# Kernel tuning notes

Measured on AMD Instinct MI355X. Metric: run time of the kernel, lower is better.

## Reference

```python
import jax, jax.numpy as jnp
import numpy as np

K = 7          # involution kernel size
GC = 16        # group_channels (hardcoded in module)
BN_EPS = 1e-5
LN_EPS = 1e-6


def _forward(x, conv1_w, conv1_b, bn_gamma, bn_beta, bn_mean, bn_var,
             conv2_w, conv2_b, ln_w, ln_b, w1, b1, w2, b2):
    b, c, h, w = x.shape
    groups = c // GC
    # --- involution: dynamic kernel generation (1x1 conv -> BN(eval) -> ReLU -> 1x1 conv) ---
    t = jnp.einsum('bchw,oc->bohw', x, conv1_w) + conv1_b[None, :, None, None]
    t = (t - bn_mean[None, :, None, None]) * (bn_gamma / jnp.sqrt(bn_var + BN_EPS))[None, :, None, None] \
        + bn_beta[None, :, None, None]
    t = jax.nn.relu(t)
    wgt = jnp.einsum('bchw,oc->bohw', t, conv2_w) + conv2_b[None, :, None, None]
    wgt = wgt.reshape(b, groups, K * K, h, w)                  # (b,g,k2,h,w)
    # --- unfold: gather kxk neighborhoods (channel-major, then kh, kw — matches torch Unfold) ---
    p = (K - 1) // 2
    xp = jnp.pad(x, ((0, 0), (0, 0), (p, p), (p, p)))
    patches = jnp.stack([xp[:, :, i:i + h, j:j + w]
                         for i in range(K) for j in range(K)], axis=2)   # (b,c,k2,h,w)
    patches = patches.reshape(b, groups, GC, K * K, h, w)
    # weighted sum over kernel positions
    out = jnp.einsum('bgkhw,bgckhw->bgchw', wgt, patches).reshape(b, c, h, w)
    # --- LN + MLP residual (channels_last) ---
    y = out.transpose(0, 2, 3, 1)                               # (b,h,w,c)
    mu = y.mean(-1, keepdims=True)
    var = ((y - mu) ** 2).mean(-1, keepdims=True)
    y = (y - mu) / jnp.sqrt(var + LN_EPS) * ln_w + ln_b
    y = jax.nn.gelu(y @ w1.T + b1, approximate=False)           # torch GELU = exact erf
    y = y @ w2.T + b2                                           # dropout_rate=0 -> identity
    return y.transpose(0, 3, 1, 2) + x


def setup_inputs() -> dict:
    key = jax.random.key(0)
    ks = jax.random.split(key, 6)
    dim = 128
    groups = dim // GC
    red = dim // 4
    b, h, w = 8, 56, 56
    return {
        'x': jax.random.normal(ks[0], (b, dim, h, w), jnp.float32),
        'conv1_w': jax.random.normal(ks[1], (red, dim), jnp.float32) * (1.0 / np.sqrt(dim)),
        'conv1_b': jnp.zeros((red,), jnp.float32),
        'bn_gamma': jnp.ones((red,), jnp.float32),
        'bn_beta': jnp.zeros((red,), jnp.float32),
        'bn_mean': jnp.zeros((red,), jnp.float32),
        'bn_var': jnp.ones((red,), jnp.float32),
        'conv2_w': jax.random.normal(ks[2], (K * K * groups, red), jnp.float32) * (1.0 / np.sqrt(red)),
        'conv2_b': jnp.zeros((K * K * groups,), jnp.float32),
        'ln_w': jnp.ones((dim,), jnp.float32),
        'ln_b': jnp.zeros((dim,), jnp.float32),
        'w1': jax.random.normal(ks[3], (4 * dim, dim), jnp.float32) * (1.0 / np.sqrt(dim)),
        'b1': jnp.zeros((4 * dim,), jnp.float32),
        'w2': jax.random.normal(ks[4], (dim, 4 * dim), jnp.float32) * (1.0 / np.sqrt(4 * dim)),
        'b2': jnp.zeros((dim,), jnp.float32),
    }


def reference(x, conv1_w, conv1_b, bn_gamma, bn_beta, bn_mean, bn_var,
              conv2_w, conv2_b, ln_w, ln_b, w1, b1, w2, b2):
    return _forward(x, conv1_w, conv1_b, bn_gamma, bn_beta, bn_mean, bn_var,
                    conv2_w, conv2_b, ln_w, ln_b, w1, b1, w2, b2)
```

## Files before the change

### kernel.cpp

```cpp
#include <hip/hip_runtime.h>
#include <hip/hip_bf16.h>
#include <math.h>

#define HW    3136
#define WIMG  56
#define NPIX  25088
#define CIN   128
#define RED   32
#define NGROUP 8
#define GCH   16
#define KKK   49

typedef __attribute__((ext_vector_type(8))) short short8;
typedef __attribute__((ext_vector_type(4))) float f32x4;
typedef unsigned short ushort_t;

static __device__ __forceinline__ unsigned int f2b(float f) {
    union { __hip_bfloat16 b; unsigned short u; } cv;
    cv.b = __float2bfloat16(f);
    return (unsigned int)cv.u;
}

static __device__ __forceinline__ float gelu_t(float h) {
    float z = h * fmaf(0.0356774081f, h * h, 0.7978845608f);
    float e = __expf(-2.f * z);
    return __fdividef(h, 1.f + e);
}

__global__ __launch_bounds__(256) void k_prep(const float* __restrict__ conv1_w,
    const float* __restrict__ conv1_b, const float* __restrict__ bn_g,
    const float* __restrict__ bn_b, const float* __restrict__ bn_m,
    const float* __restrict__ bn_v, const float* __restrict__ conv2_w,
    const float* __restrict__ ln_w, const float* __restrict__ w1,
    const float* __restrict__ w2,
    ushort_t* __restrict__ c1b, ushort_t* __restrict__ c2b,
    ushort_t* __restrict__ lw1b, ushort_t* __restrict__ w2b,
    float* __restrict__ sc1, float* __restrict__ sh1)
{
    int id = blockIdx.x * 256 + threadIdx.x;
    w2b[id] = (ushort_t)f2b(w2[id]);
    int c = id & 127;
    lw1b[id] = (ushort_t)f2b(w1[id] * ln_w[c]);
    if (id < 4096)  c1b[id] = (ushort_t)f2b(conv1_w[id]);
    if (id < 12800) c2b[id] = (id < 12544) ? (ushort_t)f2b(conv2_w[id]) : (ushort_t)0;
    if (id < 32) {
        float sc = bn_g[id] * rsqrtf(bn_v[id] + 1e-5f);
        sc1[id] = sc;
        sh1[id] = (conv1_b[id] - bn_m[id]) * sc + bn_b[id];
    }
}

__global__ void k_prep2(const float* __restrict__ w1, const float* __restrict__ ln_w,
    const float* __restrict__ ln_b, const float* __restrict__ b1,
    float* __restrict__ s1, float* __restrict__ t1)
{
    int n = threadIdx.x;
    const float* wr = w1 + (size_t)n * 128;
    float s = 0.f, t = 0.f;
    #pragma unroll 8
    for (int c = 0; c < 128; ++c) { float w = wr[c]; s += ln_w[c] * w; t += ln_b[c] * w; }
    s1[n] = s; t1[n] = t + b1[n];
}

__global__ __launch_bounds__(256) void k_dw(const float* __restrict__ x,
    const short* __restrict__ c1b, const short* __restrict__ c2b,
    const float* __restrict__ sc1, const float* __restrict__ sh1,
    const float* __restrict__ c2bias, ushort_t* __restrict__ wgtT)
{
    __shared__ short sxa[64 * 136];
    __shared__ short st[64 * 40];
    int tid = threadIdx.x;
    int P0 = blockIdx.x * 64;
    int b  = P0 / HW;
    int p0 = P0 - b * HW;
    const float* xb = x + (size_t)b * CIN * HW + p0;
    #pragma unroll
    for (int it = 0; it < 32; ++it) {
        int idx = it * 256 + tid;
        int c = idx >> 6, pp = idx & 63;
        sxa[pp * 136 + c] = (short)f2b(xb[(size_t)c * HW + pp]);
    }
    __syncthreads();
    int lane = tid & 63, wv = tid >> 6;
    int ln15 = lane & 15, quad = lane >> 4;

    f32x4 acc1[2] = {(f32x4)0.f, (f32x4)0.f};
    #pragma unroll
    for (int kc = 0; kc < 128; kc += 32) {
        short8 af = *(const short8*)&sxa[(wv * 16 + ln15) * 136 + kc + quad * 8];
        #pragma unroll
        for (int nt = 0; nt < 2; ++nt) {
            short8 bf = *(const short8*)&c1b[(size_t)(nt * 16 + ln15) * 128 + kc + quad * 8];
            acc1[nt] = __builtin_amdgcn_mfma_f32_16x16x32_bf16(af, bf, acc1[nt], 0, 0, 0);
        }
    }
    #pragma unroll
    for (int nt = 0; nt < 2; ++nt) {
        int o = nt * 16 + ln15;
        float sc = sc1[o], sh = sh1[o];
        #pragma unroll
        for (int r = 0; r < 4; ++r) {
            float tv = fmaxf(acc1[nt][r] * sc + sh, 0.f);
            st[(wv * 16 + quad * 4 + r) * 40 + o] = (short)f2b(tv);
        }
    }
    short8 af2 = *(const short8*)&st[(wv * 16 + ln15) * 40 + quad * 8];
    f32x4 zc = (f32x4)0.f;
    #pragma unroll
    for (int nt = 0; nt < 25; ++nt) {
        int gk = nt * 16 + ln15;
        short8 bf2 = *(const short8*)&c2b[(size_t)gk * 32 + quad * 8];
        f32x4 a2 = __builtin_amdgcn_mfma_f32_16x16x32_bf16(af2, bf2, zc, 0, 0, 0);
        if (gk < 392) {
            float bj = c2bias[gk];
            uint2 pk;
            pk.x = f2b(a2[0] + bj) | (f2b(a2[1] + bj) << 16);
            pk.y = f2b(a2[2] + bj) | (f2b(a2[3] + bj) << 16);
            *(uint2*)&wgtT[(size_t)gk * NPIX + P0 + wv * 16 + quad * 4] = pk;
        }
    }
}

__global__ __launch_bounds__(256) void k_inv(const float* __restrict__ x,
    const ushort_t* __restrict__ wgtT, ushort_t* __restrict__ invb)
{
    int id  = blockIdx.x * 256 + threadIdx.x;
    int gy  = id / 6272;
    int q   = id - gy * 6272;
    int g   = gy >> 1;
    int sub = gy & 1;
    int P0  = q * 4;
    int b   = P0 / HW;
    int p   = P0 - b * HW;
    int prow = p / WIMG;
    int pcol = p - prow * WIMG;
    const float* xc = x + ((size_t)b * CIN + g * GCH + sub * 8) * HW;
    const ushort_t* wg = wgtT + (size_t)g * KKK * NPIX + P0;
    float acc[4][8];
    #pragma unroll
    for (int i = 0; i < 4; ++i)
        #pragma unroll
        for (int c = 0; c < 8; ++c) acc[i][c] = 0.f;
    bool c_lo = (pcol >= 4);
    bool c_hi = (pcol <= 48);
    #pragma unroll
    for (int dy = -3; dy <= 3; ++dy) {
        int grow = prow + dy;
        if (grow < 0 || grow >= WIMG) continue;
        float wkf[7][4];
        #pragma unroll
        for (int dx = 0; dx < 7; ++dx) {
            uint2 wld = *(const uint2*)&wg[(size_t)((dy + 3) * 7 + dx) * NPIX];
            wkf[dx][0] = __uint_as_float(wld.x << 16);
            wkf[dx][1] = __uint_as_float(wld.x & 0xffff0000u);
            wkf[dx][2] = __uint_as_float(wld.y << 16);
            wkf[dx][3] = __uint_as_float(wld.y & 0xffff0000u);
        }
        const float* xrow = xc + grow * WIMG + pcol;
        #pragma unroll
        for (int c = 0; c < 8; ++c) {
            const float* xr = xrow + (size_t)c * HW;
            float4 v0 = c_lo ? *(const float4*)(xr - 4) : make_float4(0.f,0.f,0.f,0.f);
            float4 v1 = *(const float4*)(xr);
            float4 v2 = c_hi ? *(const float4*)(xr + 4) : make_float4(0.f,0.f,0.f,0.f);
            float vv[12] = {v0.x,v0.y,v0.z,v0.w, v1.x,v1.y,v1.z,v1.w, v2.x,v2.y,v2.z,v2.w};
            #pragma unroll
            for (int dx = 0; dx < 7; ++dx)
                #pragma unroll
                for (int i = 0; i < 4; ++i)
                    acc[i][c] += wkf[dx][i] * vv[i + dx + 1];
        }
    }
    #pragma unroll
    for (int i = 0; i < 4; ++i) {
        unsigned pk[4];
        #pragma unroll
        for (int h = 0; h < 4; ++h)
            pk[h] = f2b(acc[i][2*h]) | (f2b(acc[i][2*h+1]) << 16);
        *(uint4*)&invb[(size_t)(P0 + i) * CIN + g * GCH + sub * 8] = make_uint4(pk[0],pk[1],pk[2],pk[3]);
    }
}

__global__ __launch_bounds__(256) void k_stats(const ushort_t* __restrict__ invb,
    float* __restrict__ ssum, float* __restrict__ ssq)
{
    int p = blockIdx.x * 256 + threadIdx.x;
    const uint4* row = (const uint4*)(invb + (size_t)p * CIN);
    float s = 0.f, s2 = 0.f;
    #pragma unroll
    for (int i = 0; i < 16; ++i) {
        uint4 v = row[i];
        unsigned u[4] = {v.x, v.y, v.z, v.w};
        #pragma unroll
        for (int j = 0; j < 4; ++j) {
            float f0 = __uint_as_float(u[j] << 16);
            float f1 = __uint_as_float(u[j] & 0xffff0000u);
            s += f0 + f1;
            s2 += f0 * f0 + f1 * f1;
        }
    }
    ssum[p] = s; ssq[p] = s2;
}

__global__ __launch_bounds__(256) void k_mlp(const ushort_t* __restrict__ invb,
    const ushort_t* __restrict__ lw1b, const ushort_t* __restrict__ w2b,
    const float* __restrict__ ssum, const float* __restrict__ ssq,
    const float* __restrict__ s1, const float* __restrict__ t1,
    const float* __restrict__ b2, const float* __restrict__ xres,
    float* __restrict__ outp)
{
    __shared__ short sx[64 * 136];
    __shared__ short sh[64 * 136];
    __shared__ float sls[512], slt[512];
    int tid = threadIdx.x;
    int P0  = blockIdx.x * 64;

    #pragma unroll
    for (int it = 0; it < 4; ++it) {
        int idx = it * 256 + tid;
        int row = idx >> 4, ch = idx & 15;
        *(uint4*)&sx[row * 136 + ch * 8] =
            *(const uint4*)&invb[(size_t)(P0 + row) * 128 + ch * 8];
    }
    sls[tid] = s1[tid]; sls[tid + 256] = s1[tid + 256];
    slt[tid] = t1[tid]; slt[tid + 256] = t1[tid + 256];
    __syncthreads();

    int lane = tid & 63, wv = tid >> 6;
    int ln15 = lane & 15, quad = lane >> 4;

    float mu_r[4], rs_r[4];
    #pragma unroll
    for (int tn = 0; tn < 4; ++tn) {
        int p = P0 + tn * 16 + ln15;
        float m = ssum[p] * (1.f / 128.f);
        float v = ssq[p] * (1.f / 128.f) - m * m;
        mu_r[tn] = m; rs_r[tn] = rsqrtf(v + 1e-6f);
    }

    f32x4 acc2[4][2];
    #pragma unroll
    for (int i = 0; i < 4; ++i)
        #pragma unroll
        for (int j = 0; j < 2; ++j) acc2[i][j] = (f32x4)0.f;

    for (int j = 0; j < 4; ++j) {
        f32x4 acc1[2][4];
        #pragma unroll
        for (int tm = 0; tm < 2; ++tm)
            #pragma unroll
            for (int tn = 0; tn < 4; ++tn) acc1[tm][tn] = (f32x4)0.f;
        #pragma unroll
        for (int kc = 0; kc < 128; kc += 32) {
            short8 af[2], bf[4];
            #pragma unroll
            for (int tm = 0; tm < 2; ++tm)
                af[tm] = *(const short8*)&lw1b[(size_t)(j * 128 + wv * 32 + tm * 16 + ln15) * 128 + kc + quad * 8];
            #pragma unroll
            for (int tn = 0; tn < 4; ++tn)
                bf[tn] = *(const short8*)&sx[(tn * 16 + ln15) * 136 + kc + quad * 8];
            #pragma unroll
            for (int tm = 0; tm < 2; ++tm)
                #pragma unroll
                for (int tn = 0; tn < 4; ++tn)
                    acc1[tm][tn] = __builtin_amdgcn_mfma_f32_16x16x32_bf16(af[tm], bf[tn], acc1[tm][tn], 0, 0, 0);
        }
        #pragma unroll
        for (int tn = 0; tn < 4; ++tn) {
            int px = tn * 16 + ln15;
            #pragma unroll
            for (int tm = 0; tm < 2; ++tm) {
                int nl = wv * 32 + tm * 16 + quad * 4;
                int n  = j * 128 + nl;
                float g0 = gelu_t(rs_r[tn] * (acc1[tm][tn][0] - mu_r[tn] * sls[n + 0]) + slt[n + 0]);
                float g1 = gelu_t(rs_r[tn] * (acc1[tm][tn][1] - mu_r[tn] * sls[n + 1]) + slt[n + 1]);
                float g2 = gelu_t(rs_r[tn] * (acc1[tm][tn][2] - mu_r[tn] * sls[n + 2]) + slt[n + 2]);
                float g3 = gelu_t(rs_r[tn] * (acc1[tm][tn][3] - mu_r[tn] * sls[n + 3]) + slt[n + 3]);
                uint2 pk;
                pk.x = f2b(g0) | (f2b(g1) << 16);
                pk.y = f2b(g2) | (f2b(g3) << 16);
                *(uint2*)&sh[px * 136 + nl] = pk;
            }
        }
        __syncthreads();
        #pragma unroll
        for (int kc = 0; kc < 128; kc += 32) {
            short8 af[4], bf[2];
            #pragma unroll
            for (int tm = 0; tm < 4; ++tm)
                af[tm] = *(const short8*)&sh[(tm * 16 + ln15) * 136 + kc + quad * 8];
            #pragma unroll
            for (int tn = 0; tn < 2; ++tn)
                bf[tn] = *(const short8*)&w2b[(size_t)(wv * 32 + tn * 16 + ln15) * 512 + j * 128 + kc + quad * 8];
            #pragma unroll
            for (int tm = 0; tm < 4; ++tm)
                #pragma unroll
                for (int tn = 0; tn < 2; ++tn)
                    acc2[tm][tn] = __builtin_amdgcn_mfma_f32_16x16x32_bf16(af[tm], bf[tn], acc2[tm][tn], 0, 0, 0);
        }
        __syncthreads();
    }

    int b = P0 / HW, p0i = P0 - b * HW;
    #pragma unroll
    for (int tm = 0; tm < 4; ++tm) {
        int p = p0i + tm * 16 + quad * 4;
        #pragma unroll
        for (int tn = 0; tn < 2; ++tn) {
            int c = wv * 32 + tn * 16 + ln15;
            size_t base = ((size_t)b * CIN + c) * HW + p;
            float bj = b2[c];
            float4 rv = *(const float4*)&xres[base];
            float4 ov = make_float4(acc2[tm][tn][0] + bj + rv.x,
                                    acc2[tm][tn][1] + bj + rv.y,
                                    acc2[tm][tn][2] + bj + rv.z,
                                    acc2[tm][tn][3] + bj + rv.w);
            *(float4*)&outp[base] = ov;
        }
    }
}

extern "C" void kernel_launch(void* const* d_in, const int* in_sizes, int n_in,
                              void* d_out, int out_size, void* d_ws, size_t ws_size,
                              hipStream_t stream) {
    const float* x       = (const float*)d_in[0];
    const float* conv1_w = (const float*)d_in[1];
    const float* conv1_b = (const float*)d_in[2];
    const float* bn_g    = (const float*)d_in[3];
    const float* bn_b    = (const float*)d_in[4];
    const float* bn_m    = (const float*)d_in[5];
    const float* bn_v    = (const float*)d_in[6];
    const float* conv2_w = (const float*)d_in[7];
    const float* conv2_b = (const float*)d_in[8];
    const float* ln_w    = (const float*)d_in[9];
    const float* ln_b    = (const float*)d_in[10];
    const float* w1      = (const float*)d_in[11];
    const float* b1      = (const float*)d_in[12];
    const float* w2      = (const float*)d_in[13];
    const float* b2      = (const float*)d_in[14];
    float* out = (float*)d_out;

    float* F = (float*)d_ws;
    float* ssum = F;
    float* ssq  = F + 25088;
    float* sc1  = F + 50176;
    float* sh1  = F + 50208;
    float* s1   = F + 50240;
    float* t1   = F + 50752;
    ushort_t* S    = (ushort_t*)(F + 51264);
    ushort_t* wgtT = S;
    ushort_t* invb = S + 9834496;
    ushort_t* c1b  = invb + 3211264;
    ushort_t* c2b  = c1b + 4096;
    ushort_t* lw1b = c2b + 12800;
    ushort_t* w2b  = lw1b + 65536;

    k_prep <<<256, 256, 0, stream>>>(conv1_w, conv1_b, bn_g, bn_b, bn_m, bn_v,
                                     conv2_w, ln_w, w1, w2, c1b, c2b, lw1b, w2b, sc1, sh1);
    k_prep2<<<1, 512, 0, stream>>>(w1, ln_w, ln_b, b1, s1, t1);
    k_dw   <<<392, 256, 0, stream>>>(x, (const short*)c1b, (const short*)c2b,
                                     sc1, sh1, conv2_b, wgtT);
    k_inv  <<<392, 256, 0, stream>>>(x, wgtT, invb);
    k_stats<<<98, 256, 0, stream>>>(invb, ssum, ssq);
    k_mlp  <<<392, 256, 0, stream>>>(invb, lw1b, w2b, ssum, ssq, s1, t1, b2, x, out);
}
```

Before: 172.8 us.

## Fuse kernel-gen, involution, LN stats and MLP into one megakernel

Merges the dynamic-weight generation, involution, LayerNorm statistics and MLP kernels into a single per-64-pixel-tile kernel. The generated weights and involution outputs stay in shared memory, so the large global intermediates (wgtT, invb, ssum/ssq) and three launches go away. LN statistics are reduced in shared memory from fp32 accumulators instead of being reread from bf16. The cost is about 78KB of shared memory per block, which lowers occupancy, and the involution stage of each block now runs serially before the MLP stage.

New measurement: 149.9 us. 1.15x faster.

```diff
diff --git a/kernel.cpp b/kernel.cpp
--- a/kernel.cpp
+++ b/kernel.cpp
@@ -62,45 +62,57 @@
     s1[n] = s; t1[n] = t + b1[n];
 }
 
-__global__ __launch_bounds__(256) void k_dw(const float* __restrict__ x,
+__global__ __launch_bounds__(256) void k_mega(const float* __restrict__ x,
     const short* __restrict__ c1b, const short* __restrict__ c2b,
     const float* __restrict__ sc1, const float* __restrict__ sh1,
-    const float* __restrict__ c2bias, ushort_t* __restrict__ wgtT)
+    const float* __restrict__ c2bias,
+    const ushort_t* __restrict__ lw1b, const ushort_t* __restrict__ w2b,
+    const float* __restrict__ s1, const float* __restrict__ t1,
+    const float* __restrict__ b2, float* __restrict__ outp)
 {
-    __shared__ short sxa[64 * 136];
-    __shared__ short st[64 * 40];
-    int tid = threadIdx.x;
-    int P0 = blockIdx.x * 64;
-    int b  = P0 / HW;
-    int p0 = P0 - b * HW;
-    const float* xb = x + (size_t)b * CIN * HW + p0;
+    __shared__ __align__(16) char smem[79936];
+    short* swg  = (short*)smem;
+    short* sh   = (short*)smem;
+    short* sx   = (short*)smem + 26656;
+    short* st   = (short*)(smem + 70720);
+    float* sred  = (float*)(smem + 70720);
+    float* sred2 = sred + 1088;
+    float* smu   = sred2 + 1088;
+    float* srs   = smu + 64;
+
+    int tid  = threadIdx.x;
+    int P0   = blockIdx.x * 64;
+    int b    = P0 / HW;
+    int p0i  = P0 - b * HW;
+    int lane = tid & 63, wv = tid >> 6;
+    int ln15 = lane & 15, quad = lane >> 4;
+
+    const float* xb = x + (size_t)b * CIN * HW + p0i;
     #pragma unroll
     for (int it = 0; it < 32; ++it) {
         int idx = it * 256 + tid;
         int c = idx >> 6, pp = idx & 63;
-        sxa[pp * 136 + c] = (short)f2b(xb[(size_t)c * HW + pp]);
+        sx[pp * 136 + c] = (short)f2b(xb[(size_t)c * HW + pp]);
     }
     __syncthreads();
-    int lane = tid & 63, wv = tid >> 6;
-    int ln15 = lane & 15, quad = lane >> 4;
-
-    f32x4 acc1[2] = {(f32x4)0.f, (f32x4)0.f};
+
+    f32x4 acc1c[2] = {(f32x4)0.f, (f32x4)0.f};
     #pragma unroll
     for (int kc = 0; kc < 128; kc += 32) {
-        short8 af = *(const short8*)&sxa[(wv * 16 + ln15) * 136 + kc + quad * 8];
+        short8 af = *(const short8*)&sx[(wv * 16 + ln15) * 136 + kc + quad * 8];
         #pragma unroll
         for (int nt = 0; nt < 2; ++nt) {
             short8 bf = *(const short8*)&c1b[(size_t)(nt * 16 + ln15) * 128 + kc + quad * 8];
-            acc1[nt] = __builtin_amdgcn_mfma_f32_16x16x32_bf16(af, bf, acc1[nt], 0, 0, 0);
+            acc1c[nt] = __builtin_amdgcn_mfma_f32_16x16x32_bf16(af, bf, acc1c[nt], 0, 0, 0);
         }
     }
     #pragma unroll
     for (int nt = 0; nt < 2; ++nt) {
         int o = nt * 16 + ln15;
-        float sc = sc1[o], sh = sh1[o];
+        float sc = sc1[o], shv = sh1[o];
         #pragma unroll
         for (int r = 0; r < 4; ++r) {
-            float tv = fmaxf(acc1[nt][r] * sc + sh, 0.f);
+            float tv = fmaxf(acc1c[nt][r] * sc + shv, 0.f);
             st[(wv * 16 + quad * 4 + r) * 40 + o] = (short)f2b(tv);
         }
     }
@@ -116,126 +128,90 @@
             uint2 pk;
             pk.x = f2b(a2[0] + bj) | (f2b(a2[1] + bj) << 16);
             pk.y = f2b(a2[2] + bj) | (f2b(a2[3] + bj) << 16);
-            *(uint2*)&wgtT[(size_t)gk * NPIX + P0 + wv * 16 + quad * 4] = pk;
-        }
-    }
-}
-
-__global__ __launch_bounds__(256) void k_inv(const float* __restrict__ x,
-    const ushort_t* __restrict__ wgtT, ushort_t* __restrict__ invb)
-{
-    int id  = blockIdx.x * 256 + threadIdx.x;
-    int gy  = id / 6272;
-    int q   = id - gy * 6272;
-    int g   = gy >> 1;
-    int sub = gy & 1;
-    int P0  = q * 4;
-    int b   = P0 / HW;
-    int p   = P0 - b * HW;
-    int prow = p / WIMG;
-    int pcol = p - prow * WIMG;
-    const float* xc = x + ((size_t)b * CIN + g * GCH + sub * 8) * HW;
-    const ushort_t* wg = wgtT + (size_t)g * KKK * NPIX + P0;
-    float acc[4][8];
-    #pragma unroll
-    for (int i = 0; i < 4; ++i)
-        #pragma unroll
-        for (int c = 0; c < 8; ++c) acc[i][c] = 0.f;
-    bool c_lo = (pcol >= 4);
-    bool c_hi = (pcol <= 48);
-    #pragma unroll
-    for (int dy = -3; dy <= 3; ++dy) {
-        int grow = prow + dy;
-        if (grow < 0 || grow >= WIMG) continue;
-        float wkf[7][4];
-        #pragma unroll
-        for (int dx = 0; dx < 7; ++dx) {
-            uint2 wld = *(const uint2*)&wg[(size_t)((dy + 3) * 7 + dx) * NPIX];
-            wkf[dx][0] = __uint_as_float(wld.x << 16);
-            wkf[dx][1] = __uint_as_float(wld.x & 0xffff0000u);
-            wkf[dx][2] = __uint_as_float(wld.y << 16);
-            wkf[dx][3] = __uint_as_float(wld.y & 0xffff0000u);
-        }
-        const float* xrow = xc + grow * WIMG + pcol;
-        #pragma unroll
-        for (int c = 0; c < 8; ++c) {
-            const float* xr = xrow + (size_t)c * HW;
-            float4 v0 = c_lo ? *(const float4*)(xr - 4) : make_float4(0.f,0.f,0.f,0.f);
-            float4 v1 = *(const float4*)(xr);
-            float4 v2 = c_hi ? *(const float4*)(xr + 4) : make_float4(0.f,0.f,0.f,0.f);
-            float vv[12] = {v0.x,v0.y,v0.z,v0.w, v1.x,v1.y,v1.z,v1.w, v2.x,v2.y,v2.z,v2.w};
-            #pragma unroll
-            for (int dx = 0; dx < 7; ++dx)
+            *(uint2*)&swg[gk * 68 + wv * 16 + quad * 4] = pk;
+        }
+    }
+    __syncthreads();
+
+    {
+        int q   = tid & 15;
+        int gy  = tid >> 4;
+        int g   = gy >> 1;
+        int sub = gy & 1;
+        int pl0 = q * 4;
+        int p   = p0i + pl0;
+        int prow = p / WIMG;
+        int pcol = p - prow * WIMG;
+        const float* xc = x + ((size_t)b * CIN + g * GCH + sub * 8) * HW;
+        float acc[4][8];
+        #pragma unroll
+        for (int i = 0; i < 4; ++i)
+            #pragma unroll
+            for (int c = 0; c < 8; ++c) acc[i][c] = 0.f;
+        bool c_lo = (pcol >= 4);
+        bool c_hi = (pcol <= 48);
+        #pragma unroll
+        for (int dy = -3; dy <= 3; ++dy) {
+            int grow = prow + dy;
+            if (grow < 0 || grow >= WIMG) continue;
+            float wkf[7][4];
+            #pragma unroll
+            for (int dx = 0; dx < 7; ++dx) {
+                int gk = g * KKK + (dy + 3) * 7 + dx;
+                uint2 wld = *(const uint2*)&swg[gk * 68 + pl0];
+                wkf[dx][0] = __uint_as_float(wld.x << 16);
+                wkf[dx][1] = __uint_as_float(wld.x & 0xffff0000u);
+                wkf[dx][2] = __uint_as_float(wld.y << 16);
+                wkf[dx][3] = __uint_as_float(wld.y & 0xffff0000u);
+            }
+            const float* xrow = xc + grow * WIMG + pcol;
+            #pragma unroll
+            for (int c = 0; c < 8; ++c) {
+                const float* xr = xrow + (size_t)c * HW;
+                float4 v0 = c_lo ? *(const float4*)(xr - 4) : make_float4(0.f,0.f,0.f,0.f);
+                float4 v1 = *(const float4*)(xr);
+                float4 v2 = c_hi ? *(const float4*)(xr + 4) : make_float4(0.f,0.f,0.f,0.f);
+                float vv[12] = {v0.x,v0.y,v0.z,v0.w, v1.x,v1.y,v1.z,v1.w, v2.x,v2.y,v2.z,v2.w};
                 #pragma unroll
-                for (int i = 0; i < 4; ++i)
-                    acc[i][c] += wkf[dx][i] * vv[i + dx + 1];
-        }
-    }
-    #pragma unroll
-    for (int i = 0; i < 4; ++i) {
-        unsigned pk[4];
-        #pragma unroll
-        for (int h = 0; h < 4; ++h)
-            pk[h] = f2b(acc[i][2*h]) | (f2b(acc[i][2*h+1]) << 16);
-        *(uint4*)&invb[(size_t)(P0 + i) * CIN + g * GCH + sub * 8] = make_uint4(pk[0],pk[1],pk[2],pk[3]);
-    }
-}
-
-__global__ __launch_bounds__(256) void k_stats(const ushort_t* __restrict__ invb,
-    float* __restrict__ ssum, float* __restrict__ ssq)
-{
-    int p = blockIdx.x * 256 + threadIdx.x;
-    const uint4* row = (const uint4*)(invb + (size_t)p * CIN);
-    float s = 0.f, s2 = 0.f;
-    #pragma unroll
-    for (int i = 0; i < 16; ++i) {
-        uint4 v = row[i];
-        unsigned u[4] = {v.x, v.y, v.z, v.w};
-        #pragma unroll
-        for (int j = 0; j < 4; ++j) {
-            float f0 = __uint_as_float(u[j] << 16);
-            float f1 = __uint_as_float(u[j] & 0xffff0000u);
-            s += f0 + f1;
-            s2 += f0 * f0 + f1 * f1;
-        }
-    }
-    ssum[p] = s; ssq[p] = s2;
-}
-
-__global__ __launch_bounds__(256) void k_mlp(const ushort_t* __restrict__ invb,
-    const ushort_t* __restrict__ lw1b, const ushort_t* __restrict__ w2b,
-    const float* __restrict__ ssum, const float* __restrict__ ssq,
-    const float* __restrict__ s1, const float* __restrict__ t1,
-    const float* __restrict__ b2, const float* __restrict__ xres,
-    float* __restrict__ outp)
-{
-    __shared__ short sx[64 * 136];
-    __shared__ short sh[64 * 136];
-    __shared__ float sls[512], slt[512];
-    int tid = threadIdx.x;
-    int P0  = blockIdx.x * 64;
-
-    #pragma unroll
-    for (int it = 0; it < 4; ++it) {
-        int idx = it * 256 + tid;
-        int row = idx >> 4, ch = idx & 15;
-        *(uint4*)&sx[row * 136 + ch * 8] =
-            *(const uint4*)&invb[(size_t)(P0 + row) * 128 + ch * 8];
-    }
-    sls[tid] = s1[tid]; sls[tid + 256] = s1[tid + 256];
-    slt[tid] = t1[tid]; slt[tid + 256] = t1[tid + 256];
+                for (int dx = 0; dx < 7; ++dx)
+                    #pragma unroll
+                    for (int i = 0; i < 4; ++i)
+                        acc[i][c] += wkf[dx][i] * vv[i + dx + 1];
+            }
+        }
+        #pragma unroll
+        for (int i = 0; i < 4; ++i) {
+            unsigned pk[4];
+            float s = 0.f, s2 = 0.f;
+            #pragma unroll
+            for (int h = 0; h < 4; ++h)
+                pk[h] = f2b(acc[i][2*h]) | (f2b(acc[i][2*h+1]) << 16);
+            #pragma unroll
+            for (int c = 0; c < 8; ++c) { s += acc[i][c]; s2 += acc[i][c] * acc[i][c]; }
+            *(uint4*)&sx[(pl0 + i) * 136 + g * 16 + sub * 8] = make_uint4(pk[0],pk[1],pk[2],pk[3]);
+            sred [(pl0 + i) * 17 + gy] = s;
+            sred2[(pl0 + i) * 17 + gy] = s2;
+        }
+    }
     __syncthreads();
 
-    int lane = tid & 63, wv = tid >> 6;
-    int ln15 = lane & 15, quad = lane >> 4;
+    if (tid < 64) {
+        float s = 0.f, s2 = 0.f;
+        #pragma unroll
+        for (int gy = 0; gy < 16; ++gy) { s += sred[tid * 17 + gy]; s2 += sred2[tid * 17 + gy]; }
+        float m = s * (1.f / 128.f);
+        float v = s2 * (1.f / 128.f) - m * m;
+        smu[tid] = m;
+        srs[tid] = rsqrtf(v + 1e-6f);
+    }
+    __syncthreads();
 
     float mu_r[4], rs_r[4];
     #pragma unroll
     for (int tn = 0; tn < 4; ++tn) {
-        int p = P0 + tn * 16 + ln15;
-        float m = ssum[p] * (1.f / 128.f);
-        float v = ssq[p] * (1.f / 128.f) - m * m;
-        mu_r[tn] = m; rs_r[tn] = rsqrtf(v + 1e-6f);
+        int px = tn * 16 + ln15;
+        mu_r[tn] = smu[px];
+        rs_r[tn] = srs[px];
     }
 
     f32x4 acc2[4][2];
@@ -266,16 +242,18 @@
                     acc1[tm][tn] = __builtin_amdgcn_mfma_f32_16x16x32_bf16(af[tm], bf[tn], acc1[tm][tn], 0, 0, 0);
         }
         #pragma unroll
-        for (int tn = 0; tn < 4; ++tn) {
-            int px = tn * 16 + ln15;
-            #pragma unroll
-            for (int tm = 0; tm < 2; ++tm) {
-                int nl = wv * 32 + tm * 16 + quad * 4;
-                int n  = j * 128 + nl;
-                float g0 = gelu_t(rs_r[tn] * (acc1[tm][tn][0] - mu_r[tn] * sls[n + 0]) + slt[n + 0]);
-                float g1 = gelu_t(rs_r[tn] * (acc1[tm][tn][1] - mu_r[tn] * sls[n + 1]) + slt[n + 1]);
-                float g2 = gelu_t(rs_r[tn] * (acc1[tm][tn][2] - mu_r[tn] * sls[n + 2]) + slt[n + 2]);
-                float g3 = gelu_t(rs_r[tn] * (acc1[tm][tn][3] - mu_r[tn] * sls[n + 3]) + slt[n + 3]);
+        for (int tm = 0; tm < 2; ++tm) {
+            int nl = wv * 32 + tm * 16 + quad * 4;
+            int n  = j * 128 + nl;
+            float4 s14 = *(const float4*)&s1[n];
+            float4 t14 = *(const float4*)&t1[n];
+            #pragma unroll
+            for (int tn = 0; tn < 4; ++tn) {
+                int px = tn * 16 + ln15;
+                float g0 = gelu_t(rs_r[tn] * (acc1[tm][tn][0] - mu_r[tn] * s14.x) + t14.x);
+                float g1 = gelu_t(rs_r[tn] * (acc1[tm][tn][1] - mu_r[tn] * s14.y) + t14.y);
+                float g2 = gelu_t(rs_r[tn] * (acc1[tm][tn][2] - mu_r[tn] * s14.z) + t14.z);
+                float g3 = gelu_t(rs_r[tn] * (acc1[tm][tn][3] - mu_r[tn] * s14.w) + t14.w);
                 uint2 pk;
                 pk.x = f2b(g0) | (f2b(g1) << 16);
                 pk.y = f2b(g2) | (f2b(g3) << 16);
@@ -301,7 +279,6 @@
         __syncthreads();
     }
 
-    int b = P0 / HW, p0i = P0 - b * HW;
     #pragma unroll
     for (int tm = 0; tm < 4; ++tm) {
         int p = p0i + tm * 16 + quad * 4;
@@ -310,7 +287,7 @@
             int c = wv * 32 + tn * 16 + ln15;
             size_t base = ((size_t)b * CIN + c) * HW + p;
             float bj = b2[c];
-            float4 rv = *(const float4*)&xres[base];
+            float4 rv = *(const float4*)&x[base];
             float4 ov = make_float4(acc2[tm][tn][0] + bj + rv.x,
                                     acc2[tm][tn][1] + bj + rv.y,
                                     acc2[tm][tn][2] + bj + rv.z,
@@ -341,16 +318,12 @@
     float* out = (float*)d_out;
 
     float* F = (float*)d_ws;
-    float* ssum = F;
-    float* ssq  = F + 25088;
-    float* sc1  = F + 50176;
-    float* sh1  = F + 50208;
-    float* s1   = F + 50240;
-    float* t1   = F + 50752;
-    ushort_t* S    = (ushort_t*)(F + 51264);
-    ushort_t* wgtT = S;
-    ushort_t* invb = S + 9834496;
-    ushort_t* c1b  = invb + 3211264;
+    float* sc1  = F;
+    float* sh1  = F + 32;
+    float* s1   = F + 64;
+    float* t1   = F + 576;
+    ushort_t* S    = (ushort_t*)(F + 1088);
+    ushort_t* c1b  = S;
     ushort_t* c2b  = c1b + 4096;
     ushort_t* lw1b = c2b + 12800;
     ushort_t* w2b  = lw1b + 65536;
@@ -358,9 +331,6 @@
     k_prep <<<256, 256, 0, stream>>>(conv1_w, conv1_b, bn_g, bn_b, bn_m, bn_v,
                                      conv2_w, ln_w, w1, w2, c1b, c2b, lw1b, w2b, sc1, sh1);
     k_prep2<<<1, 512, 0, stream>>>(w1, ln_w, ln_b, b1, s1, t1);
-    k_dw   <<<392, 256, 0, stream>>>(x, (const short*)c1b, (const short*)c2b,
-                                     sc1, sh1, conv2_b, wgtT);
-    k_inv  <<<392, 256, 0, stream>>>(x, wgtT, invb);
-    k_stats<<<98, 256, 0, stream>>>(invb, ssum, ssq);
-    k_mlp  <<<392, 256, 0, stream>>>(invb, lw1b, w2b, ssum, ssq, s1, t1, b2, x, out);
-}
+    k_mega <<<392, 256, 0, stream>>>(x, (const short*)c1b, (const short*)c2b,
+                                     sc1, sh1, conv2_b, lw1b, w2b, s1, t1, b2, out);
+}
```
